# Optimization experiments

Measured on AMD Instinct MI355X. Metric: run time of the kernel, lower is better.

## Reference

```python
import jax, jax.numpy as jnp
import numpy as np

D_MODEL = 272
D_STATE = 32
N_LAYERS = 12
D_INNER = 2 * D_MODEL      # expand=2 (mamba_ssm default)
D_CONV = 4                 # mamba_ssm default
DT_RANK = (D_MODEL + 15) // 16  # ceil(272/16) = 17
B_SZ = 2
SEQ = 512


def setup_inputs() -> dict:
    key = jax.random.key(0)
    ks = jax.random.split(key, 16)
    rn = lambda k, shape, s=0.02: jax.random.normal(k, shape, jnp.float32) * s
    # dt bias init: softplus^{-1} of dt in [1e-3, 0.1] (mamba-style)
    dt0 = jax.random.uniform(ks[6], (N_LAYERS, 2, D_INNER), jnp.float32, 1e-3, 0.1)
    a_log = jnp.broadcast_to(jnp.log(jnp.arange(1, D_STATE + 1, dtype=jnp.float32)),
                             (N_LAYERS, 2, D_INNER, D_STATE))
    return {
        "x": jax.random.normal(ks[0], (B_SZ, SEQ, D_MODEL), jnp.float32),
        "y": jax.random.uniform(ks[1], (B_SZ, 1), jnp.float32),
        "in_proj_w": rn(ks[2], (N_LAYERS, 2, 2 * D_INNER, D_MODEL)),
        "conv_w": rn(ks[3], (N_LAYERS, 2, D_INNER, D_CONV), 0.1),
        "conv_b": jnp.zeros((N_LAYERS, 2, D_INNER), jnp.float32),
        "x_proj_w": rn(ks[4], (N_LAYERS, 2, DT_RANK + 2 * D_STATE, D_INNER)),
        "dt_proj_w": rn(ks[5], (N_LAYERS, 2, D_INNER, DT_RANK), 0.1),
        "dt_proj_b": jnp.log(jnp.expm1(dt0)),
        "A_log": a_log,
        "Dskip": jnp.ones((N_LAYERS, 2, D_INNER), jnp.float32),
        "out_proj_w": rn(ks[7], (N_LAYERS, 2, D_MODEL, D_INNER)),
        "lambda_q1": rn(ks[8], (N_LAYERS, D_MODEL), 0.05),
        "norm1_w": jnp.ones((N_LAYERS, D_MODEL), jnp.float32),
        "norm2_w": jnp.ones((N_LAYERS, D_MODEL), jnp.float32),
        "mlp_w": rn(ks[9], (D_MODEL, D_MODEL)),
        "mlp_b": jnp.zeros((D_MODEL,), jnp.float32),
        "predict_w": rn(ks[10], (1, D_MODEL + 1)),
        "predict_b": jnp.zeros((1,), jnp.float32),
    }


def _rmsnorm(x, w, eps=1e-5):
    return x * jax.lax.rsqrt(jnp.mean(x * x, axis=-1, keepdims=True) + eps) * w


def _mamba(x, p):
    """Single-direction Mamba block. x: (B, L, D_MODEL)."""
    in_w, cw, cb, xw, dtw, dtb, a_log, dskip, ow = p
    bsz = x.shape[0]
    xz = jnp.einsum('bld,ed->ble', x, in_w)            # (B,L,2*D_INNER)
    xin, z = jnp.split(xz, 2, axis=-1)
    # causal depthwise conv1d, kernel 4
    xc = jax.lax.conv_general_dilated(
        xin.transpose(0, 2, 1), cw[:, None, :], (1,), [(D_CONV - 1, 0)],
        feature_group_count=D_INNER, dimension_numbers=('NCL', 'OIL', 'NCL'))
    xc = jax.nn.silu(xc + cb[:, None]).transpose(0, 2, 1)  # (B,L,D_INNER)
    dbc = jnp.einsum('bld,ed->ble', xc, xw)
    dt, Bm, Cm = jnp.split(dbc, [DT_RANK, DT_RANK + D_STATE], axis=-1)
    dt = jax.nn.softplus(jnp.einsum('blr,dr->bld', dt, dtw) + dtb)  # (B,L,D_INNER)
    A = -jnp.exp(a_log)                                  # (D_INNER, D_STATE)

    @jax.checkpoint
    def step(h, inp):
        dt_t, x_t, B_t, C_t = inp                        # (B,Din),(B,Din),(B,Ds),(B,Ds)
        h = jnp.exp(dt_t[..., None] * A) * h + (dt_t * x_t)[..., None] * B_t[:, None, :]
        return h, jnp.einsum('bds,bs->bd', h, C_t)

    h0 = jnp.zeros((bsz, D_INNER, D_STATE), x.dtype)
    xs = (dt.transpose(1, 0, 2), xc.transpose(1, 0, 2),
          Bm.transpose(1, 0, 2), Cm.transpose(1, 0, 2))
    _, ys = jax.lax.scan(step, h0, xs)                   # ys: (L,B,D_INNER)
    yo = ys.transpose(1, 0, 2) + dskip * xc
    yo = yo * jax.nn.silu(z)
    return jnp.einsum('bld,od->blo', yo, ow)


def _forward(x, y, in_proj_w, conv_w, conv_b, x_proj_w, dt_proj_w, dt_proj_b,
             A_log, Dskip, out_proj_w, lambda_q1, norm1_w, norm2_w,
             mlp_w, mlp_b, predict_w, predict_b):
    mats = (in_proj_w, conv_w, conv_b, x_proj_w, dt_proj_w, dt_proj_b, A_log, Dskip, out_proj_w)
    for i in range(N_LAYERS):
        lam_init = 0.8 - 0.6 * np.exp(-0.3 * i)
        xn = _rmsnorm(x, norm1_w[i])
        lam_full = jax.nn.sigmoid(jnp.sum(lambda_q1[i])) + lam_init
        y1 = _mamba(xn, tuple(a[i, 0] for a in mats))
        y2 = jnp.flip(_mamba(jnp.flip(xn, 1), tuple(a[i, 1] for a in mats)), 1)
        attn = _rmsnorm(y1 - lam_full * y2, norm2_w[i])
        x = x + attn * (1.0 - lam_init)
    x2 = jax.nn.relu(jnp.mean(x, axis=1) @ mlp_w.T + mlp_b)
    feats = jnp.concatenate([x2, y], axis=-1)
    logits = feats @ predict_w.T + predict_b
    return logits, x2


def reference(x, y, in_proj_w, conv_w, conv_b, x_proj_w, dt_proj_w, dt_proj_b,
              A_log, Dskip, out_proj_w, lambda_q1, norm1_w, norm2_w,
              mlp_w, mlp_b, predict_w, predict_b):
    return _forward(x, y, in_proj_w, conv_w, conv_b, x_proj_w, dt_proj_w, dt_proj_b,
                    A_log, Dskip, out_proj_w, lambda_q1, norm1_w, norm2_w,
                    mlp_w, mlp_b, predict_w, predict_b)
```

## Files before the change

### kernel.cpp

```cpp
#include <hip/hip_runtime.h>
#include <math.h>

#define DM   272
#define DS   32
#define DI   544
#define DTR  17
#define SEQL 512
#define NB   2
#define ROWS 1024
#define DXZ  1088
#define NL   12
#define KP   288

typedef unsigned short ushort_t;
typedef __attribute__((ext_vector_type(8))) short bx8;
typedef __attribute__((ext_vector_type(4))) float fx4;

#define OFF_X     0
#define OFF_XZ    279552
#define OFF_XCT   2507776
#define OFF_DTT   3621888
#define OFF_ZT    4736000
#define OFF_BM    5850112
#define OFF_CM    5915648
#define OFF_YOT   5981184
#define OFF_Y12   7095296
#define OFF_XMP   7652352
#define OFF_DTWT  7656704
#define OFF_XNH   7878656
#define OFF_XNL   8026112
#define OFF_YTMH  8173568
#define OFF_YTML  8730624
#define OFF_WINH  9287680
#define OFF_WINL  13047808
#define OFF_WOUTH 16807936
#define OFF_WOUTL 18583552

#define NINW  (12*2176*KP)
#define NOUTW (12*544*544)

__device__ __forceinline__ float sigmoid_fast(float x){ return 1.f/(1.f+__expf(-x)); }
__device__ __forceinline__ float softplus_f(float x){ return (x > 20.f) ? x : log1pf(__expf(x)); }

__device__ __forceinline__ void bf16split(float x, ushort_t& h, ushort_t& l){
  unsigned uh = __float_as_uint(x) & 0xffff0000u;
  h = (ushort_t)(uh >> 16);
  float r = x - __uint_as_float(uh);
  l = (ushort_t)(__float_as_uint(r) >> 16);
}

__device__ __forceinline__ float block_reduce_256(float v, volatile float* sred, int tid){
#pragma unroll
  for (int m=32; m>=1; m>>=1) v += __shfl_xor(v, m);
  __syncthreads();
  if ((tid & 63) == 0) sred[tid>>6] = v;
  __syncthreads();
  return sred[0]+sred[1]+sred[2]+sred[3];
}

__global__ __launch_bounds__(256) void k_convw(const float* __restrict__ inw,
    const float* __restrict__ outw,
    ushort_t* __restrict__ winh, ushort_t* __restrict__ winl,
    ushort_t* __restrict__ wouth, ushort_t* __restrict__ woutl)
{
  int idx = blockIdx.x*256 + threadIdx.x;
  if (idx < NINW){
    int k = idx % KP; int row = idx / KP;
    float v = (k < DM) ? inw[(size_t)row*DM + k] : 0.f;
    ushort_t h,l; bf16split(v,h,l);
    winh[idx]=h; winl[idx]=l;
  } else if (idx < NINW + NOUTW){
    int j = idx - NINW;
    float v = outw[j];
    ushort_t h,l; bf16split(v,h,l);
    wouth[j]=h; woutl[j]=l;
  }
}

__global__ __launch_bounds__(256) void k_transpose(const float* __restrict__ dtw,
                                                   float* __restrict__ dtwT){
  int idx = blockIdx.x*256 + threadIdx.x;
  const int T2 = 24*544*DTR;
  if (idx < T2){
    int ld = idx / (544*DTR); int rem = idx - ld*(544*DTR);
    int d = rem / DTR; int r = rem - d*DTR;
    dtwT[(size_t)ld*DTR*544 + (size_t)r*544 + d] = dtw[idx];
  }
}

__global__ __launch_bounds__(64) void k_init(const float* __restrict__ x0,
                                             const float* __restrict__ n1w0,
                                             float* __restrict__ xb,
                                             ushort_t* __restrict__ xnh, ushort_t* __restrict__ xnl){
  int r = blockIdx.x, tid = threadIdx.x;
  float vv[5]; float ss = 0.f;
#pragma unroll
  for (int i=0;i<5;i++){
    int c = tid + i*64; float v = 0.f;
    if (c < DM){ v = x0[(size_t)r*DM+c]; xb[(size_t)r*DM+c]=v; }
    vv[i]=v; ss += v*v;
  }
#pragma unroll
  for (int m=32;m>=1;m>>=1) ss += __shfl_xor(ss,m);
  float ivr = rsqrtf(ss*(1.f/DM)+1e-5f);
#pragma unroll
  for (int i=0;i<5;i++){
    int c = tid + i*64;
    if (c < DM){
      ushort_t h,l; bf16split(vv[i]*ivr*n1w0[c],h,l);
      xnh[(size_t)r*KP+c]=h; xnl[(size_t)r*KP+c]=l;
    }
  }
  if (tid < 16){ xnh[(size_t)r*KP+DM+tid]=0; xnl[(size_t)r*KP+DM+tid]=0; }
}

__global__ __launch_bounds__(256) void k_gin(
  const ushort_t* __restrict__ xnh, const ushort_t* __restrict__ xnl,
  const ushort_t* __restrict__ wh,  const ushort_t* __restrict__ wl,
  float* __restrict__ xz)
{
  const int tid = threadIdx.x;
  const int wv = tid >> 6, lane = tid & 63;
  const int m16 = lane & 15, quad = lane >> 4;
  const int q8 = quad << 3;
  const int m0 = blockIdx.x << 6;
  const int nt = blockIdx.y;
  const int dir = (nt >= 17) ? 1 : 0;
  const int n0l = (nt - dir*17) << 6;
  const int ncol = n0l + (wv<<4) + m16;
  const ushort_t* bhp = wh + (size_t)(dir*1088 + ncol)*KP + q8;
  const ushort_t* blp = wl + (size_t)(dir*1088 + ncol)*KP + q8;
  const ushort_t* ahp = xnh + (size_t)(m0 + m16)*KP + q8;
  const ushort_t* alp = xnl + (size_t)(m0 + m16)*KP + q8;
  fx4 acc[4];
#pragma unroll
  for (int mt=0;mt<4;mt++) acc[mt] = (fx4){0.f,0.f,0.f,0.f};
  for (int k0=0;k0<KP;k0+=32){
    bx8 bh = *(const bx8*)(bhp + k0);
    bx8 bl = *(const bx8*)(blp + k0);
#pragma unroll
    for (int mt=0;mt<4;mt++){
      bx8 ah = *(const bx8*)(ahp + (size_t)mt*16*KP + k0);
      bx8 al = *(const bx8*)(alp + (size_t)mt*16*KP + k0);
      acc[mt] = __builtin_amdgcn_mfma_f32_16x16x32_bf16(ah, bh, acc[mt], 0,0,0);
      acc[mt] = __builtin_amdgcn_mfma_f32_16x16x32_bf16(al, bh, acc[mt], 0,0,0);
      acc[mt] = __builtin_amdgcn_mfma_f32_16x16x32_bf16(ah, bl, acc[mt], 0,0,0);
    }
  }
#pragma unroll
  for (int mt=0;mt<4;mt++){
#pragma unroll
    for (int r=0;r<4;r++){
      int rg = m0 + mt*16 + quad*4 + r;
      int b = rg >> 9, t = rg & 511;
      int ts = dir ? (511 - t) : t;
      xz[((size_t)((dir*NB + b)*SEQL + ts))*DXZ + ncol] = acc[mt][r];
    }
  }
}

__global__ __launch_bounds__(512) void k_xdt(
  const float* __restrict__ xz, const float* __restrict__ cwl, const float* __restrict__ cbl,
  const float* __restrict__ xwl, const float* __restrict__ dtwTl, const float* __restrict__ dtbl,
  float* __restrict__ xcT, float* __restrict__ dtT, float* __restrict__ zT,
  float* __restrict__ Bmg, float* __restrict__ Cmg)
{
  __shared__ float xcs[8][548];
  __shared__ float part[8][8][82];
  __shared__ float dts[8][DTR];
  const int tid = threadIdx.x;
  const int blk = blockIdx.x;
  const int seg = blk >> 6;
  const int dir = seg >> 1;
  const int t0 = (blk & 63) << 3;
  const float* xzb  = xz + (size_t)seg*SEQL*DXZ;
  const float* cw   = cwl + dir*DI*4;
  const float* cb   = cbl + dir*DI;
  const float* xw   = xwl + (size_t)dir*81*DI;
  const float* dtwT = dtwTl + (size_t)dir*DTR*DI;
  const float* dtb  = dtbl + dir*DI;
  const size_t chb = (size_t)seg*DI;

  for (int j = tid; j < DI; j += 512){
    float4 w4 = *(const float4*)(cw + j*4);
    float bj = cb[j];
    float xv[11];
#pragma unroll
    for (int q=0; q<11; q++){
      int t = t0 + q - 3;
      xv[q] = (t >= 0) ? xzb[(size_t)t*DXZ + j] : 0.f;
    }
    float xo[8], zo[8];
#pragma unroll
    for (int rr=0; rr<8; rr++){
      float acc = bj + w4.x*xv[rr] + w4.y*xv[rr+1] + w4.z*xv[rr+2] + w4.w*xv[rr+3];
      float v = acc * sigmoid_fast(acc);
      xcs[rr][j] = v; xo[rr] = v;
      zo[rr] = xzb[(size_t)(t0+rr)*DXZ + 544 + j];
    }
    float* xr = xcT + (chb + j)*SEQL + t0;
    *(float4*)(xr)   = make_float4(xo[0],xo[1],xo[2],xo[3]);
    *(float4*)(xr+4) = make_float4(xo[4],xo[5],xo[6],xo[7]);
    float* zr = zT + (chb + j)*SEQL + t0;
    *(float4*)(zr)   = make_float4(zo[0],zo[1],zo[2],zo[3]);
    *(float4*)(zr+4) = make_float4(zo[4],zo[5],zo[6],zo[7]);
  }
  __syncthreads();

  if (tid < 328){
    const int i = tid >> 3, ks = tid & 7;
    const int e0 = 2*i;
    const int e1r = (e0+1 < 81) ? (e0+1) : 80;
    const int kb = ks*68;
    const float* w0 = xw + (size_t)e0*DI + kb;
    const float* w1 = xw + (size_t)e1r*DI + kb;
    float acc0[8], acc1[8];
#pragma unroll
    for (int rr=0; rr<8; rr++){ acc0[rr]=0.f; acc1[rr]=0.f; }
    for (int k=0; k<68; k+=4){
      float4 wa = *(const float4*)(w0 + k);
      float4 wb = *(const float4*)(w1 + k);
#pragma unroll
      for (int rr=0; rr<8; rr++){
        float4 x4 = *(const float4*)(&xcs[rr][kb + k]);
        acc0[rr] = fmaf(wa.x,x4.x, fmaf(wa.y,x4.y, fmaf(wa.z,x4.z, fmaf(wa.w,x4.w, acc0[rr]))));
        acc1[rr] = fmaf(wb.x,x4.x, fmaf(wb.y,x4.y, fmaf(wb.z,x4.z, fmaf(wb.w,x4.w, acc1[rr]))));
      }
    }
#pragma unroll
    for (int rr=0; rr<8; rr++){
      part[ks][rr][e0]   = acc0[rr];
      part[ks][rr][e0+1] = acc1[rr];
    }
  }
  __syncthreads();

  for (int idx=tid; idx<648; idx+=512){
    int ta = idx / 81, e = idx - ta*81;
    float s = 0.f;
#pragma unroll
    for (int ks=0; ks<8; ks++) s += part[ks][ta][e];
    size_t row = (size_t)seg*SEQL + t0 + ta;
    if (e < DTR)      dts[ta][e] = s;
    else if (e < 49)  Bmg[row*DS + (e-DTR)] = s;
    else              Cmg[row*DS + (e-49)] = s;
  }
  __syncthreads();

  {
    const int c1 = tid;
    const bool h2 = tid < 32; const int c2 = 512 + tid;
    float w1[DTR], w2[DTR];
#pragma unroll
    for (int q=0; q<DTR; q++){
      w1[q] = dtwT[q*DI + c1];
      w2[q] = h2 ? dtwT[q*DI + c2] : 0.f;
    }
    float b1 = dtb[c1], b2 = h2 ? dtb[c2] : 0.f;
    float o1[8], o2[8];
#pragma unroll
    for (int rr=0; rr<8; rr++){
      float a1=b1, a2=b2;
#pragma unroll
      for (int q=0; q<DTR; q++){
        float dv = dts[rr][q];
        a1 = fmaf(w1[q],dv,a1); a2 = fmaf(w2[q],dv,a2);
      }
      o1[rr]=softplus_f(a1); o2[rr]=softplus_f(a2);
    }
    float* r1 = dtT + (chb + c1)*SEQL + t0;
    *(float4*)(r1)   = make_float4(o1[0],o1[1],o1[2],o1[3]);
    *(float4*)(r1+4) = make_float4(o1[4],o1[5],o1[6],o1[7]);
    if (h2){
      float* r2 = dtT + (chb + c2)*SEQL + t0;
      *(float4*)(r2)   = make_float4(o2[0],o2[1],o2[2],o2[3]);
      *(float4*)(r2+4) = make_float4(o2[4],o2[5],o2[6],o2[7]);
    }
  }
}

__global__ __launch_bounds__(128) void k_scan(
  const float* __restrict__ dtT, const float* __restrict__ xcT,
  const float* __restrict__ Bmg, const float* __restrict__ Cmg,
  const float* __restrict__ alogl, const float* __restrict__ dskl,
  const float* __restrict__ zT, float* __restrict__ yoT)
{
  __shared__ float hl[16][33], pl[16][33], Hi[16][33];
  const int d = blockIdx.x, b = blockIdx.y, dir = blockIdx.z;
  const int seg = dir*NB + b;
  const int tid = threadIdx.x;
  const int c = tid >> 3, sg = tid & 7, s0 = sg << 2;
  float A0,A1,A2,A3;
  {
    const float* al = alogl + (size_t)(dir*DI + d)*DS + s0;
    A0 = -expf(al[0]); A1 = -expf(al[1]); A2 = -expf(al[2]); A3 = -expf(al[3]);
  }
  const size_t cr = ((size_t)seg*DI + d)*SEQL;
  const float* dtr = dtT + cr;
  const float* xcr = xcT + cr;
  const float* zr  = zT  + cr;
  float* yor = yoT + cr;
  const float* Bp = Bmg + (size_t)seg*SEQL*DS + s0;
  const float* Cp = Cmg + (size_t)seg*SEQL*DS + s0;
  float h0=0,h1=0,h2=0,h3=0,p0=1,p1=1,p2=1,p3=1;
  const int tb = c << 5;
  for (int tq=0; tq<8; tq++){
    const int t4 = tb + (tq<<2);
    float4 dt4 = *(const float4*)(dtr + t4);
    const float* dtp4 = (const float*)&dt4;
    float4 xc4 = *(const float4*)(xcr + t4);
    const float* xcp4 = (const float*)&xc4;
#pragma unroll
    for (int u=0; u<4; u++){
      float ldt = dtp4[u], lxc = xcp4[u];
      float4 B4 = *(const float4*)(Bp + (size_t)(t4+u)*DS);
      float uu = ldt*lxc;
      float e;
      e = __expf(ldt*A0); h0 = fmaf(e,h0,uu*B4.x); p0*=e;
      e = __expf(ldt*A1); h1 = fmaf(e,h1,uu*B4.y); p1*=e;
      e = __expf(ldt*A2); h2 = fmaf(e,h2,uu*B4.z); p2*=e;
      e = __expf(ldt*A3); h3 = fmaf(e,h3,uu*B4.w); p3*=e;
    }
  }
  hl[c][s0]=h0; hl[c][s0+1]=h1; hl[c][s0+2]=h2; hl[c][s0+3]=h3;
  pl[c][s0]=p0; pl[c][s0+1]=p1; pl[c][s0+2]=p2; pl[c][s0+3]=p3;
  __syncthreads();
  if (tid < 32){
    float H = 0.f;
    Hi[0][tid] = 0.f;
    for (int cc=1; cc<16; cc++){
      H = fmaf(pl[cc-1][tid], H, hl[cc-1][tid]);
      Hi[cc][tid] = H;
    }
  }
  __syncthreads();
  h0=Hi[c][s0]; h1=Hi[c][s0+1]; h2=Hi[c][s0+2]; h3=Hi[c][s0+3];
  const float dsk = dskl[dir*DI + d];
  for (int tq=0; tq<8; tq++){
    const int t4 = tb + (tq<<2);
    float4 dt4 = *(const float4*)(dtr + t4);
    const float* dtp4 = (const float*)&dt4;
    float4 xc4 = *(const float4*)(xcr + t4);
    const float* xcp4 = (const float*)&xc4;
    float4 z4 = *(const float4*)(zr + t4);
    const float* zp4 = (const float*)&z4;
    float yv[4];
#pragma unroll
    for (int u=0; u<4; u++){
      float ldt = dtp4[u], lxc = xcp4[u];
      float4 B4 = *(const float4*)(Bp + (size_t)(t4+u)*DS);
      float4 C4 = *(const float4*)(Cp + (size_t)(t4+u)*DS);
      float uu = ldt*lxc;
      float e;
      e = __expf(ldt*A0); h0 = fmaf(e,h0,uu*B4.x);
      e = __expf(ldt*A1); h1 = fmaf(e,h1,uu*B4.y);
      e = __expf(ldt*A2); h2 = fmaf(e,h2,uu*B4.z);
      e = __expf(ldt*A3); h3 = fmaf(e,h3,uu*B4.w);
      float y = h0*C4.x + h1*C4.y + h2*C4.z + h3*C4.w;
      y += __shfl_xor(y,1); y += __shfl_xor(y,2); y += __shfl_xor(y,4);
      float z = zp4[u];
      yv[u] = fmaf(dsk, lxc, y) * (z * sigmoid_fast(z));
    }
    if (sg==0) *(float4*)(yor + t4) = make_float4(yv[0],yv[1],yv[2],yv[3]);
  }
}

__global__ __launch_bounds__(256) void k_yotm(const float* __restrict__ yoT,
                                              ushort_t* __restrict__ ytmh,
                                              ushort_t* __restrict__ ytml){
  __shared__ float tl[32][65];
  const int tid = threadIdx.x;
  const int d0 = blockIdx.x << 5;
  const int t0 = blockIdx.y << 6;
  const int seg = blockIdx.z;
  const int ty = tid >> 4, tx = tid & 15;
#pragma unroll
  for (int p=0; p<2; p++){
    int d = p*16 + ty;
    float4 v = *(const float4*)(yoT + ((size_t)(seg*DI + d0 + d))*SEQL + t0 + tx*4);
    tl[d][tx*4+0]=v.x; tl[d][tx*4+1]=v.y; tl[d][tx*4+2]=v.z; tl[d][tx*4+3]=v.w;
  }
  __syncthreads();
  const int tloc = tid >> 2, dq = (tid & 3) << 3;
  ushort_t h[8], l[8];
#pragma unroll
  for (int j=0;j<8;j++) bf16split(tl[dq+j][tloc], h[j], l[j]);
  uint4 ph, pl4;
  ph.x = (unsigned)h[0] | ((unsigned)h[1]<<16);
  ph.y = (unsigned)h[2] | ((unsigned)h[3]<<16);
  ph.z = (unsigned)h[4] | ((unsigned)h[5]<<16);
  ph.w = (unsigned)h[6] | ((unsigned)h[7]<<16);
  pl4.x = (unsigned)l[0] | ((unsigned)l[1]<<16);
  pl4.y = (unsigned)l[2] | ((unsigned)l[3]<<16);
  pl4.z = (unsigned)l[4] | ((unsigned)l[5]<<16);
  pl4.w = (unsigned)l[6] | ((unsigned)l[7]<<16);
  size_t base = ((size_t)(seg*SEQL + t0 + tloc))*DI + d0 + dq;
  *(uint4*)(ytmh + base) = ph;
  *(uint4*)(ytml + base) = pl4;
}

__global__ __launch_bounds__(256) void k_gout(
  const ushort_t* __restrict__ ath, const ushort_t* __restrict__ atl,
  const ushort_t* __restrict__ wh,  const ushort_t* __restrict__ wl,
  float* __restrict__ y12)
{
  const int tid = threadIdx.x;
  const int wv = tid >> 6, lane = tid & 63;
  const int m16 = lane & 15, quad = lane >> 4;
  const int q8 = quad << 3;
  const int m0 = blockIdx.x << 6;
  const int dir = blockIdx.z;
  const int nloc = (blockIdx.y << 6) + (wv<<4) + m16;
  const bool nval = nloc < DM;
  const int nrow = dir*DM + (nval ? nloc : (DM-1));
  const int bseg = m0 >> 9;
  const int tr0 = m0 & 511;
  const int seg = dir*NB + bseg;
  const ushort_t* bhp = wh + (size_t)nrow*DI + q8;
  const ushort_t* blp = wl + (size_t)nrow*DI + q8;
  const ushort_t* ahp = ath + ((size_t)(seg*SEQL) + tr0 + m16)*DI + q8;
  const ushort_t* alp = atl + ((size_t)(seg*SEQL) + tr0 + m16)*DI + q8;
  fx4 acc[4];
#pragma unroll
  for (int mt=0;mt<4;mt++) acc[mt] = (fx4){0.f,0.f,0.f,0.f};
  for (int k0=0;k0<DI;k0+=32){
    bx8 bh = *(const bx8*)(bhp + k0);
    bx8 bl = *(const bx8*)(blp + k0);
#pragma unroll
    for (int mt=0;mt<4;mt++){
      bx8 ah = *(const bx8*)(ahp + (size_t)mt*16*DI + k0);
      bx8 al = *(const bx8*)(alp + (size_t)mt*16*DI + k0);
      acc[mt] = __builtin_amdgcn_mfma_f32_16x16x32_bf16(ah, bh, acc[mt], 0,0,0);
      acc[mt] = __builtin_amdgcn_mfma_f32_16x16x32_bf16(al, bh, acc[mt], 0,0,0);
      acc[mt] = __builtin_amdgcn_mfma_f32_16x16x32_bf16(ah, bl, acc[mt], 0,0,0);
    }
  }
  if (nval){
#pragma unroll
    for (int mt=0;mt<4;mt++){
#pragma unroll
      for (int r=0;r<4;r++){
        int rg = m0 + mt*16 + quad*4 + r;
        int b = rg >> 9, t = rg & 511;
        int ts = dir ? (511 - t) : t;
        y12[(size_t)dir*ROWS*DM + ((size_t)(b*SEQL + ts))*DM + nloc] = acc[mt][r];
      }
    }
  }
}

__global__ __launch_bounds__(256) void k_combine(
  const float* __restrict__ y12, const float* __restrict__ lamq,
  const float* __restrict__ n2w, float* __restrict__ xb,
  const float* __restrict__ n1wn, ushort_t* __restrict__ xnh, ushort_t* __restrict__ xnl,
  float lam_init, float omli)
{
  __shared__ float sred[4];
  const int tid = threadIdx.x;
  const int r = blockIdx.x;
  const float* y1 = y12 + (size_t)r*DM;
  const float* y2 = y12 + (size_t)ROWS*DM + (size_t)r*DM;
  float lp = lamq[tid];
  if (tid < 16) lp += lamq[tid+256];
  float lsum = block_reduce_256(lp, sred, tid);
  float lam = sigmoid_fast(lsum) + lam_init;
  float a0 = y1[tid] - lam*y2[tid];
  float a1 = 0.f;
  if (tid<16) a1 = y1[tid+256] - lam*y2[tid+256];
  float ss = block_reduce_256(a0*a0 + a1*a1, sred, tid);
  float rms = rsqrtf(ss*(1.f/DM) + 1e-5f);
  float xo0 = xb[(size_t)r*DM + tid] + a0*rms*n2w[tid]*omli;
  float xo1 = 0.f;
  if (tid<16) xo1 = xb[(size_t)r*DM + tid+256] + a1*rms*n2w[tid+256]*omli;
  xb[(size_t)r*DM+tid] = xo0;
  if (tid<16) xb[(size_t)r*DM+tid+256] = xo1;
  float ss2 = block_reduce_256(xo0*xo0 + xo1*xo1, sred, tid);
  float ivn = rsqrtf(ss2*(1.f/DM) + 1e-5f);
  {
    ushort_t h,l; bf16split(xo0*ivn*n1wn[tid], h, l);
    xnh[(size_t)r*KP + tid] = h; xnl[(size_t)r*KP + tid] = l;
  }
  if (tid < 16){
    ushort_t h,l; bf16split(xo1*ivn*n1wn[tid+256], h, l);
    xnh[(size_t)r*KP + tid+256] = h; xnl[(size_t)r*KP + tid+256] = l;
    xnh[(size_t)r*KP + DM + tid] = 0; xnl[(size_t)r*KP + DM + tid] = 0;
  }
}

__global__ __launch_bounds__(256) void k_head1(const float* __restrict__ xb, float* __restrict__ xmp){
  int ch = blockIdx.x, b = blockIdx.y, tid = threadIdx.x;
  int t0 = ch*64;
  float s0=0.f, s1=0.f;
  for (int t=t0; t<t0+64; t++){
    const float* row = xb + (size_t)(b*SEQL+t)*DM;
    s0 += row[tid];
    if (tid<16) s1 += row[tid+256];
  }
  xmp[(size_t)(b*8+ch)*DM + tid] = s0;
  if (tid<16) xmp[(size_t)(b*8+ch)*DM + tid+256] = s1;
}

__global__ __launch_bounds__(256) void k_head2(
  const float* __restrict__ xmp, const float* __restrict__ yin,
  const float* __restrict__ mlpw, const float* __restrict__ mlpb,
  const float* __restrict__ pw, const float* __restrict__ pb,
  float* __restrict__ out)
{
  __shared__ float xm[2][DM];
  __shared__ float x2s[2][DM];
  __shared__ float sred[4];
  int tid = threadIdx.x;
  for (int idx=tid; idx<2*DM; idx+=256){
    int b = idx / DM, c = idx - b*DM;
    float s=0.f;
    for (int ch=0; ch<8; ch++) s += xmp[(size_t)(b*8+ch)*DM + c];
    xm[b][c] = s * (1.f/SEQL);
  }
  __syncthreads();
  for (int idx=tid; idx<2*DM; idx+=256){
    int b = idx / DM, c = idx - b*DM;
    float acc = mlpb[c];
    const float* wr = mlpw + (size_t)c*DM;
    for (int k=0;k<DM;k++) acc += wr[k]*xm[b][k];
    float v = fmaxf(acc, 0.f);
    x2s[b][c] = v;
    out[2 + b*DM + c] = v;
  }
  __syncthreads();
  for (int b=0;b<2;b++){
    float p = x2s[b][tid]*pw[tid];
    if (tid<16) p += x2s[b][tid+256]*pw[tid+256];
    float tot = block_reduce_256(p, sred, tid);
    if (tid==0) out[b] = tot + yin[b]*pw[DM] + pb[0];
  }
}

extern "C" void kernel_launch(void* const* d_in, const int* in_sizes, int n_in,
                              void* d_out, int out_size, void* d_ws, size_t ws_size,
                              hipStream_t stream)
{
  const float* x0     = (const float*)d_in[0];
  const float* yin    = (const float*)d_in[1];
  const float* in_w   = (const float*)d_in[2];
  const float* conv_w = (const float*)d_in[3];
  const float* conv_b = (const float*)d_in[4];
  const float* x_w    = (const float*)d_in[5];
  const float* dt_w   = (const float*)d_in[6];
  const float* dt_b   = (const float*)d_in[7];
  const float* a_log  = (const float*)d_in[8];
  const float* dskip  = (const float*)d_in[9];
  const float* out_w  = (const float*)d_in[10];
  const float* lamq   = (const float*)d_in[11];
  const float* n1w    = (const float*)d_in[12];
  const float* n2w    = (const float*)d_in[13];
  const float* mlpw   = (const float*)d_in[14];
  const float* mlpb   = (const float*)d_in[15];
  const float* pw     = (const float*)d_in[16];
  const float* pb     = (const float*)d_in[17];

  float* ws  = (float*)d_ws;
  float* xb  = ws + OFF_X;
  float* xz  = ws + OFF_XZ;
  float* xcT = ws + OFF_XCT;
  float* dtT = ws + OFF_DTT;
  float* zT  = ws + OFF_ZT;
  float* Bm  = ws + OFF_BM;
  float* Cm  = ws + OFF_CM;
  float* yoT = ws + OFF_YOT;
  float* y12 = ws + OFF_Y12;
  float* xmp = ws + OFF_XMP;
  float* dtwT= ws + OFF_DTWT;
  ushort_t* xnh  = (ushort_t*)(ws + OFF_XNH);
  ushort_t* xnl  = (ushort_t*)(ws + OFF_XNL);
  ushort_t* ytmh = (ushort_t*)(ws + OFF_YTMH);
  ushort_t* ytml = (ushort_t*)(ws + OFF_YTML);
  ushort_t* winh = (ushort_t*)(ws + OFF_WINH);
  ushort_t* winl = (ushort_t*)(ws + OFF_WINL);
  ushort_t* wouth= (ushort_t*)(ws + OFF_WOUTH);
  ushort_t* woutl= (ushort_t*)(ws + OFF_WOUTL);
  float* outp = (float*)d_out;

  k_convw<<<(NINW + NOUTW + 255)/256, 256, 0, stream>>>(in_w, out_w, winh, winl, wouth, woutl);
  k_transpose<<<(24*544*DTR + 255)/256, 256, 0, stream>>>(dt_w, dtwT);
  k_init<<<ROWS, 64, 0, stream>>>(x0, n1w, xb, xnh, xnl);
  for (int i=0;i<NL;i++){
    float lam_init = 0.8f - 0.6f*expf(-0.3f*(float)i);
    k_gin<<<dim3(16,34), 256, 0, stream>>>(xnh, xnl,
        winh + (size_t)i*2176*KP, winl + (size_t)i*2176*KP, xz);
    k_xdt<<<256, 512, 0, stream>>>(xz,
        conv_w + (size_t)i*2*DI*4, conv_b + (size_t)i*2*DI,
        x_w + (size_t)i*2*81*DI, dtwT + (size_t)i*2*DTR*DI, dt_b + (size_t)i*2*DI,
        xcT, dtT, zT, Bm, Cm);
    k_scan<<<dim3(DI,NB,2), 128, 0, stream>>>(dtT, xcT, Bm, Cm,
        a_log + (size_t)i*2*DI*DS, dskip + (size_t)i*2*DI, zT, yoT);
    k_yotm<<<dim3(17,8,4), 256, 0, stream>>>(yoT, ytmh, ytml);
    k_gout<<<dim3(16,5,2), 256, 0, stream>>>(ytmh, ytml,
        wouth + (size_t)i*544*544, woutl + (size_t)i*544*544, y12);
    k_combine<<<ROWS, 256, 0, stream>>>(y12, lamq + (size_t)i*DM, n2w + (size_t)i*DM,
        xb, n1w + (size_t)((i+1)%NL)*DM, xnh, xnl, lam_init, 1.f - lam_init);
  }
  k_head1<<<dim3(8,2), 256, 0, stream>>>(xb, xmp);
  k_head2<<<1, 256, 0, stream>>>(xmp, yin, mlpw, mlpb, pw, pb, outp);
}
```

Before: 1.390 ms.

## Fuse yoT transpose/bf16 split into out-projection GEMM and merge prep kernels

The out-projection GEMM now reads the fp32 scan output directly, splits it into bf16 hi/lo in registers, stages it through shared memory and prefetches the next k-slab. This replaces the separate transpose/convert kernel and its intermediate buffers in every layer. The three one-time prep kernels are merged into one grid-strided launch. This removes 12 launches and a round trip through global memory, but each of the 5 N-tile blocks now redoes the conversion for its A tile and adds two barriers per k step.

```diff
diff --git a/kernel.cpp b/kernel.cpp
--- a/kernel.cpp
+++ b/kernel.cpp
@@ -29,12 +29,10 @@
 #define OFF_DTWT  7656704
 #define OFF_XNH   7878656
 #define OFF_XNL   8026112
-#define OFF_YTMH  8173568
-#define OFF_YTML  8730624
-#define OFF_WINH  9287680
-#define OFF_WINL  13047808
-#define OFF_WOUTH 16807936
-#define OFF_WOUTL 18583552
+#define OFF_WINH  8173568
+#define OFF_WINL  11933696
+#define OFF_WOUTH 15693824
+#define OFF_WOUTL 17469440
 
 #define NINW  (12*2176*KP)
 #define NOUTW (12*544*544)
@@ -58,60 +56,56 @@
   return sred[0]+sred[1]+sred[2]+sred[3];
 }
 
-__global__ __launch_bounds__(256) void k_convw(const float* __restrict__ inw,
-    const float* __restrict__ outw,
+__global__ __launch_bounds__(256) void k_prep(
+    const float* __restrict__ inw, const float* __restrict__ outw,
+    const float* __restrict__ dtw, const float* __restrict__ x0,
+    const float* __restrict__ n1w0,
     ushort_t* __restrict__ winh, ushort_t* __restrict__ winl,
-    ushort_t* __restrict__ wouth, ushort_t* __restrict__ woutl)
-{
-  int idx = blockIdx.x*256 + threadIdx.x;
-  if (idx < NINW){
-    int k = idx % KP; int row = idx / KP;
-    float v = (k < DM) ? inw[(size_t)row*DM + k] : 0.f;
-    ushort_t h,l; bf16split(v,h,l);
-    winh[idx]=h; winl[idx]=l;
-  } else if (idx < NINW + NOUTW){
-    int j = idx - NINW;
-    float v = outw[j];
-    ushort_t h,l; bf16split(v,h,l);
-    wouth[j]=h; woutl[j]=l;
-  }
-}
-
-__global__ __launch_bounds__(256) void k_transpose(const float* __restrict__ dtw,
-                                                   float* __restrict__ dtwT){
-  int idx = blockIdx.x*256 + threadIdx.x;
-  const int T2 = 24*544*DTR;
-  if (idx < T2){
+    ushort_t* __restrict__ wouth, ushort_t* __restrict__ woutl,
+    float* __restrict__ dtwT, float* __restrict__ xb,
+    ushort_t* __restrict__ xnh, ushort_t* __restrict__ xnl)
+{
+  const int bid = blockIdx.x, tid = threadIdx.x;
+  for (int idx = bid*256 + tid; idx < NINW + NOUTW; idx += 1024*256){
+    if (idx < NINW){
+      int k = idx % KP; int row = idx / KP;
+      float v = (k < DM) ? inw[(size_t)row*DM + k] : 0.f;
+      ushort_t h,l; bf16split(v,h,l);
+      winh[idx]=h; winl[idx]=l;
+    } else {
+      int j = idx - NINW;
+      float v = outw[j];
+      ushort_t h,l; bf16split(v,h,l);
+      wouth[j]=h; woutl[j]=l;
+    }
+  }
+  for (int idx = bid*256 + tid; idx < 24*544*DTR; idx += 1024*256){
     int ld = idx / (544*DTR); int rem = idx - ld*(544*DTR);
     int d = rem / DTR; int r = rem - d*DTR;
     dtwT[(size_t)ld*DTR*544 + (size_t)r*544 + d] = dtw[idx];
   }
-}
-
-__global__ __launch_bounds__(64) void k_init(const float* __restrict__ x0,
-                                             const float* __restrict__ n1w0,
-                                             float* __restrict__ xb,
-                                             ushort_t* __restrict__ xnh, ushort_t* __restrict__ xnl){
-  int r = blockIdx.x, tid = threadIdx.x;
-  float vv[5]; float ss = 0.f;
-#pragma unroll
-  for (int i=0;i<5;i++){
-    int c = tid + i*64; float v = 0.f;
-    if (c < DM){ v = x0[(size_t)r*DM+c]; xb[(size_t)r*DM+c]=v; }
-    vv[i]=v; ss += v*v;
-  }
-#pragma unroll
-  for (int m=32;m>=1;m>>=1) ss += __shfl_xor(ss,m);
-  float ivr = rsqrtf(ss*(1.f/DM)+1e-5f);
-#pragma unroll
-  for (int i=0;i<5;i++){
-    int c = tid + i*64;
-    if (c < DM){
-      ushort_t h,l; bf16split(vv[i]*ivr*n1w0[c],h,l);
-      xnh[(size_t)r*KP+c]=h; xnl[(size_t)r*KP+c]=l;
-    }
-  }
-  if (tid < 16){ xnh[(size_t)r*KP+DM+tid]=0; xnl[(size_t)r*KP+DM+tid]=0; }
+  if (tid < 64){
+    const int r = bid, l = tid;
+    float vv[5]; float ss = 0.f;
+#pragma unroll
+    for (int i=0;i<5;i++){
+      int c = l + i*64; float v = 0.f;
+      if (c < DM){ v = x0[(size_t)r*DM+c]; xb[(size_t)r*DM+c]=v; }
+      vv[i]=v; ss += v*v;
+    }
+#pragma unroll
+    for (int m=32;m>=1;m>>=1) ss += __shfl_xor(ss,m);
+    float ivr = rsqrtf(ss*(1.f/DM)+1e-5f);
+#pragma unroll
+    for (int i=0;i<5;i++){
+      int c = l + i*64;
+      if (c < DM){
+        ushort_t h,lo; bf16split(vv[i]*ivr*n1w0[c],h,lo);
+        xnh[(size_t)r*KP+c]=h; xnl[(size_t)r*KP+c]=lo;
+      }
+    }
+    if (l < 16){ xnh[(size_t)r*KP+DM+l]=0; xnl[(size_t)r*KP+DM+l]=0; }
+  }
 }
 
 __global__ __launch_bounds__(256) void k_gin(
@@ -365,71 +359,64 @@
   }
 }
 
-__global__ __launch_bounds__(256) void k_yotm(const float* __restrict__ yoT,
-                                              ushort_t* __restrict__ ytmh,
-                                              ushort_t* __restrict__ ytml){
-  __shared__ float tl[32][65];
-  const int tid = threadIdx.x;
-  const int d0 = blockIdx.x << 5;
-  const int t0 = blockIdx.y << 6;
-  const int seg = blockIdx.z;
-  const int ty = tid >> 4, tx = tid & 15;
-#pragma unroll
-  for (int p=0; p<2; p++){
-    int d = p*16 + ty;
-    float4 v = *(const float4*)(yoT + ((size_t)(seg*DI + d0 + d))*SEQL + t0 + tx*4);
-    tl[d][tx*4+0]=v.x; tl[d][tx*4+1]=v.y; tl[d][tx*4+2]=v.z; tl[d][tx*4+3]=v.w;
-  }
-  __syncthreads();
-  const int tloc = tid >> 2, dq = (tid & 3) << 3;
-  ushort_t h[8], l[8];
-#pragma unroll
-  for (int j=0;j<8;j++) bf16split(tl[dq+j][tloc], h[j], l[j]);
-  uint4 ph, pl4;
-  ph.x = (unsigned)h[0] | ((unsigned)h[1]<<16);
-  ph.y = (unsigned)h[2] | ((unsigned)h[3]<<16);
-  ph.z = (unsigned)h[4] | ((unsigned)h[5]<<16);
-  ph.w = (unsigned)h[6] | ((unsigned)h[7]<<16);
-  pl4.x = (unsigned)l[0] | ((unsigned)l[1]<<16);
-  pl4.y = (unsigned)l[2] | ((unsigned)l[3]<<16);
-  pl4.z = (unsigned)l[4] | ((unsigned)l[5]<<16);
-  pl4.w = (unsigned)l[6] | ((unsigned)l[7]<<16);
-  size_t base = ((size_t)(seg*SEQL + t0 + tloc))*DI + d0 + dq;
-  *(uint4*)(ytmh + base) = ph;
-  *(uint4*)(ytml + base) = pl4;
-}
-
-__global__ __launch_bounds__(256) void k_gout(
-  const ushort_t* __restrict__ ath, const ushort_t* __restrict__ atl,
-  const ushort_t* __restrict__ wh,  const ushort_t* __restrict__ wl,
+__global__ __launch_bounds__(256) void k_gout2(
+  const float* __restrict__ yoT,
+  const ushort_t* __restrict__ wh, const ushort_t* __restrict__ wl,
   float* __restrict__ y12)
 {
+  __shared__ ushort_t ash[64][72];
+  __shared__ ushort_t asl[64][72];
   const int tid = threadIdx.x;
   const int wv = tid >> 6, lane = tid & 63;
-  const int m16 = lane & 15, quad = lane >> 4;
-  const int q8 = quad << 3;
+  const int m16 = lane & 15, quad = lane >> 4, q8 = quad << 3;
   const int m0 = blockIdx.x << 6;
+  const int n0 = blockIdx.y << 6;
   const int dir = blockIdx.z;
-  const int nloc = (blockIdx.y << 6) + (wv<<4) + m16;
+  const int seg = dir*NB + (m0 >> 9);
+  const int t0 = m0 & 511;
+  const int nloc = n0 + (wv<<4) + m16;
   const bool nval = nloc < DM;
-  const int nrow = dir*DM + (nval ? nloc : (DM-1));
-  const int bseg = m0 >> 9;
-  const int tr0 = m0 & 511;
-  const int seg = dir*NB + bseg;
+  const int nrow = dir*DM + (nval ? nloc : 0);
   const ushort_t* bhp = wh + (size_t)nrow*DI + q8;
   const ushort_t* blp = wl + (size_t)nrow*DI + q8;
-  const ushort_t* ahp = ath + ((size_t)(seg*SEQL) + tr0 + m16)*DI + q8;
-  const ushort_t* alp = atl + ((size_t)(seg*SEQL) + tr0 + m16)*DI + q8;
+  const int tt = tid & 63;
+  const int kq = tid >> 6;
+  const float* yob = yoT + (size_t)seg*DI*SEQL + t0 + tt;
   fx4 acc[4];
 #pragma unroll
   for (int mt=0;mt<4;mt++) acc[mt] = (fx4){0.f,0.f,0.f,0.f};
-  for (int k0=0;k0<DI;k0+=32){
+
+  float vbuf[8];
+#pragma unroll
+  for (int i=0;i<8;i++) vbuf[i] = yob[(size_t)(kq*8 + i)*SEQL];
+
+  for (int k0=0; k0<DI; k0+=32){
+    ushort_t h8[8], l8[8];
+#pragma unroll
+    for (int i=0;i<8;i++) bf16split(vbuf[i], h8[i], l8[i]);
+    uint4 ph, pl;
+    ph.x = (unsigned)h8[0] | ((unsigned)h8[1]<<16);
+    ph.y = (unsigned)h8[2] | ((unsigned)h8[3]<<16);
+    ph.z = (unsigned)h8[4] | ((unsigned)h8[5]<<16);
+    ph.w = (unsigned)h8[6] | ((unsigned)h8[7]<<16);
+    pl.x = (unsigned)l8[0] | ((unsigned)l8[1]<<16);
+    pl.y = (unsigned)l8[2] | ((unsigned)l8[3]<<16);
+    pl.z = (unsigned)l8[4] | ((unsigned)l8[5]<<16);
+    pl.w = (unsigned)l8[6] | ((unsigned)l8[7]<<16);
+    __syncthreads();
+    *(uint4*)(&ash[tt][kq*8]) = ph;
+    *(uint4*)(&asl[tt][kq*8]) = pl;
+    __syncthreads();
+    if (k0 + 32 < DI){
+#pragma unroll
+      for (int i=0;i<8;i++) vbuf[i] = yob[(size_t)(k0 + 32 + kq*8 + i)*SEQL];
+    }
     bx8 bh = *(const bx8*)(bhp + k0);
     bx8 bl = *(const bx8*)(blp + k0);
 #pragma unroll
     for (int mt=0;mt<4;mt++){
-      bx8 ah = *(const bx8*)(ahp + (size_t)mt*16*DI + k0);
-      bx8 al = *(const bx8*)(alp + (size_t)mt*16*DI + k0);
+      bx8 ah = *(const bx8*)(&ash[mt*16 + m16][q8]);
+      bx8 al = *(const bx8*)(&asl[mt*16 + m16][q8]);
       acc[mt] = __builtin_amdgcn_mfma_f32_16x16x32_bf16(ah, bh, acc[mt], 0,0,0);
       acc[mt] = __builtin_amdgcn_mfma_f32_16x16x32_bf16(al, bh, acc[mt], 0,0,0);
       acc[mt] = __builtin_amdgcn_mfma_f32_16x16x32_bf16(ah, bl, acc[mt], 0,0,0);
@@ -572,17 +559,14 @@
   float* dtwT= ws + OFF_DTWT;
   ushort_t* xnh  = (ushort_t*)(ws + OFF_XNH);
   ushort_t* xnl  = (ushort_t*)(ws + OFF_XNL);
-  ushort_t* ytmh = (ushort_t*)(ws + OFF_YTMH);
-  ushort_t* ytml = (ushort_t*)(ws + OFF_YTML);
   ushort_t* winh = (ushort_t*)(ws + OFF_WINH);
   ushort_t* winl = (ushort_t*)(ws + OFF_WINL);
   ushort_t* wouth= (ushort_t*)(ws + OFF_WOUTH);
   ushort_t* woutl= (ushort_t*)(ws + OFF_WOUTL);
   float* outp = (float*)d_out;
 
-  k_convw<<<(NINW + NOUTW + 255)/256, 256, 0, stream>>>(in_w, out_w, winh, winl, wouth, woutl);
-  k_transpose<<<(24*544*DTR + 255)/256, 256, 0, stream>>>(dt_w, dtwT);
-  k_init<<<ROWS, 64, 0, stream>>>(x0, n1w, xb, xnh, xnl);
+  k_prep<<<1024, 256, 0, stream>>>(in_w, out_w, dt_w, x0, n1w,
+      winh, winl, wouth, woutl, dtwT, xb, xnh, xnl);
   for (int i=0;i<NL;i++){
     float lam_init = 0.8f - 0.6f*expf(-0.3f*(float)i);
     k_gin<<<dim3(16,34), 256, 0, stream>>>(xnh, xnl,
@@ -593,8 +577,7 @@
         xcT, dtT, zT, Bm, Cm);
     k_scan<<<dim3(DI,NB,2), 128, 0, stream>>>(dtT, xcT, Bm, Cm,
         a_log + (size_t)i*2*DI*DS, dskip + (size_t)i*2*DI, zT, yoT);
-    k_yotm<<<dim3(17,8,4), 256, 0, stream>>>(yoT, ytmh, ytml);
-    k_gout<<<dim3(16,5,2), 256, 0, stream>>>(ytmh, ytml,
+    k_gout2<<<dim3(16,5,2), 256, 0, stream>>>(yoT,
         wouth + (size_t)i*544*544, woutl + (size_t)i*544*544, y12);
     k_combine<<<ROWS, 256, 0, stream>>>(y12, lamq + (size_t)i*DM, n2w + (size_t)i*DM,
         xb, n1w + (size_t)((i+1)%NL)*DM, xnh, xnl, lam_init, 1.f - lam_init);
```

After: 1.377 ms. About the same (-0.9%).
